# Performance work log

Hardware: AMD Instinct MI355X
Metric: run time of the kernel (lower is better)

Reference implementation:

```python
import jax, jax.numpy as jnp
import numpy as np

BS, D = 4096, 768

def setup_inputs() -> dict:
    key = jax.random.key(0)
    k1, k2 = jax.random.split(key)
    code_vec = jax.random.normal(k1, (BS, D), dtype=jnp.float32)
    nl_vec = jax.random.normal(k2, (BS, D), dtype=jnp.float32)
    return {"code_vec": code_vec, "nl_vec": nl_vec, "bs": BS}

def reference(code_vec, nl_vec, bs):
    # scores[i, j] = <nl_vec[i], code_vec[j]>  -- expressed as a GEMM
    scores = jnp.einsum("nd,md->nm", nl_vec, code_vec)  # [bs, bs]
    # CrossEntropyLoss with labels = arange(bs): mean of -log_softmax diagonal
    logprobs = jax.nn.log_softmax(scores, axis=-1)
    labels = jnp.arange(bs)
    loss = -jnp.mean(logprobs[labels, labels])
    return loss
```

## Files before the change

kernel.cpp:

```cpp
#include <hip/hip_runtime.h>
#include <hip/hip_bf16.h>
#include <math.h>

#define BSZ 4096
#define DIM 768
#define BK 64
#define NTILE (DIM / BK)
#define CSPLIT 16

typedef __attribute__((ext_vector_type(8))) short short8;
typedef __attribute__((ext_vector_type(4))) float f32x4;

__device__ __forceinline__ unsigned short f2bf(float f) {
  unsigned u = __float_as_uint(f);
  u += 0x7fffu + ((u >> 16) & 1u);
  return (unsigned short)(u >> 16);
}

__device__ __forceinline__ void gload16(const void* gp, const void* lp) {
  __builtin_amdgcn_global_load_lds(
      (const __attribute__((address_space(1))) unsigned int*)(size_t)gp,
      (__attribute__((address_space(3))) unsigned int*)(unsigned int)(size_t)lp,
      16, 0, 0);
}

__device__ __forceinline__ short8 lds_ld(const unsigned char* p) {
  return *(const short8*)p;
}

__device__ __forceinline__ void cstore(float* p, float v) {
  __hip_atomic_store(p, v, __ATOMIC_RELAXED, __HIP_MEMORY_SCOPE_AGENT);
}
__device__ __forceinline__ float cload(const float* p) {
  return __hip_atomic_load(p, __ATOMIC_RELAXED, __HIP_MEMORY_SCOPE_AGENT);
}

__global__ void convert_kernel(const float* __restrict__ src0,
                               const float* __restrict__ src1,
                               unsigned short* __restrict__ dst0,
                               unsigned short* __restrict__ dst1,
                               unsigned int* __restrict__ cnt)
{
  if (blockIdx.x == 0 && threadIdx.x <= CSPLIT) cnt[threadIdx.x] = 0u;
  const int n4 = (BSZ * DIM) / 4;
  int i = blockIdx.x * blockDim.x + threadIdx.x;
  const float* src;
  unsigned short* dst;
  if (i < n4) { src = src0; dst = dst0; }
  else        { src = src1; dst = dst1; i -= n4; }
  float4 v = *reinterpret_cast<const float4*>(src + (size_t)i * 4);
  ushort4 o;
  o.x = f2bf(v.x); o.y = f2bf(v.y); o.z = f2bf(v.z); o.w = f2bf(v.w);
  *reinterpret_cast<ushort4*>(dst + (size_t)i * 4) = o;
}

__global__ __launch_bounds__(512, 2)
void gemm_lse_kernel(const unsigned short* __restrict__ A,
                     const unsigned short* __restrict__ B,
                     float* __restrict__ pm, float* __restrict__ ps,
                     float* __restrict__ diag,
                     float* __restrict__ partial,
                     unsigned int* __restrict__ cnt,
                     float* __restrict__ out)
{
  __shared__ alignas(16) unsigned char smem[131072];
  const int tid  = threadIdx.x;
  const int w    = tid >> 6;
  const int lane = tid & 63;
  const int lr   = lane & 15;
  const int hi   = lane >> 4;
  const int wm   = w >> 2;
  const int wn   = w & 3;

  const int id  = blockIdx.y * 16 + blockIdx.x;
  const int xcd = id & 7, sq = id >> 3;
  const int bx  = ((xcd & 3) << 2) | (sq & 3);
  const int by  = ((xcd >> 2) << 3) | (sq >> 2);
  const int i0 = bx << 8;
  const int j0 = by << 8;

  const int fb0 = (hi ^ (lr & 7)) << 4;
  const int fb1 = ((4 + hi) ^ (lr & 7)) << 4;
  const int arowb = (wm * 128 + lr) * 128;
  const int browb = (wn * 64 + lr) * 128;

  const int srow = tid >> 3;
  const int gcol = ((tid & 7) ^ (srow & 7)) << 3;
  const unsigned short* pA = A + (size_t)(i0 + srow) * DIM + gcol;
  const unsigned short* pB = B + (size_t)(j0 + srow) * DIM + gcol;
  const int ldsbase = w << 10;

  f32x4 acc[8][4];
#pragma unroll
  for (int m = 0; m < 8; ++m)
#pragma unroll
    for (int n = 0; n < 4; ++n)
      acc[m][n] = (f32x4){0.f, 0.f, 0.f, 0.f};

#pragma unroll
  for (int q = 0; q < 4; ++q) {
    gload16(pA + (size_t)(q * 64) * DIM, smem + q * 8192 + ldsbase);
    gload16(pB + (size_t)(q * 64) * DIM, smem + 65536 + q * 8192 + ldsbase);
  }
  asm volatile("s_waitcnt vmcnt(0)" ::: "memory");
  __builtin_amdgcn_s_barrier();

#pragma unroll 2
  for (int u = 0; u < NTILE; ++u) {
    const int c = u & 1;
    const unsigned char* la = smem + c * 32768;
    const unsigned char* lb = smem + 65536 + c * 32768;
    unsigned char* na = smem + (c ^ 1) * 32768;
    unsigned char* nb = smem + 65536 + (c ^ 1) * 32768;
    const bool st = (u + 1 < NTILE);
    const size_t kn = (size_t)(u + 1) * BK;

    short8 aF[4], bF[4];

#pragma unroll
    for (int n = 0; n < 4; ++n) bF[n] = lds_ld(lb + browb + n * 2048 + fb0);
#pragma unroll
    for (int m = 0; m < 4; ++m) aF[m] = lds_ld(la + arowb + m * 2048 + fb0);
    if (st) {
      gload16(pB + kn,                     nb + ldsbase);
      gload16(pB + (size_t) 64 * DIM + kn, nb +     8192 + ldsbase);
      gload16(pB + (size_t)128 * DIM + kn, nb + 2 * 8192 + ldsbase);
      gload16(pB + (size_t)192 * DIM + kn, nb + 3 * 8192 + ldsbase);
      gload16(pA + kn,                     na + ldsbase);
      gload16(pA + (size_t)128 * DIM + kn, na + 2 * 8192 + ldsbase);
    }
    __builtin_amdgcn_s_barrier();
    asm volatile("s_waitcnt lgkmcnt(0)" ::: "memory");
    __builtin_amdgcn_s_setprio(1);
#pragma unroll
    for (int m = 0; m < 4; ++m)
#pragma unroll
      for (int n = 0; n < 4; ++n)
        acc[m][n] = __builtin_amdgcn_mfma_f32_16x16x32_bf16(aF[m], bF[n], acc[m][n], 0, 0, 0);
    __builtin_amdgcn_s_setprio(0);
    if (st) asm volatile("s_waitcnt vmcnt(6)" ::: "memory");
    else    asm volatile("s_waitcnt vmcnt(0)" ::: "memory");
    __builtin_amdgcn_s_barrier();

#pragma unroll
    for (int m = 0; m < 4; ++m) aF[m] = lds_ld(la + arowb + (4 + m) * 2048 + fb0);
    if (st) {
      gload16(pA + (size_t) 64 * DIM + kn, na +     8192 + ldsbase);
      gload16(pA + (size_t)192 * DIM + kn, na + 3 * 8192 + ldsbase);
    }
    __builtin_amdgcn_s_barrier();
    asm volatile("s_waitcnt lgkmcnt(0)" ::: "memory");
    __builtin_amdgcn_s_setprio(1);
#pragma unroll
    for (int m = 0; m < 4; ++m)
#pragma unroll
      for (int n = 0; n < 4; ++n)
        acc[4 + m][n] = __builtin_amdgcn_mfma_f32_16x16x32_bf16(aF[m], bF[n], acc[4 + m][n], 0, 0, 0);
    __builtin_amdgcn_s_setprio(0);
    __builtin_amdgcn_s_barrier();

#pragma unroll
    for (int n = 0; n < 4; ++n) bF[n] = lds_ld(lb + browb + n * 2048 + fb1);
#pragma unroll
    for (int m = 0; m < 4; ++m) aF[m] = lds_ld(la + arowb + m * 2048 + fb1);
    __builtin_amdgcn_s_barrier();
    asm volatile("s_waitcnt lgkmcnt(0)" ::: "memory");
    __builtin_amdgcn_s_setprio(1);
#pragma unroll
    for (int m = 0; m < 4; ++m)
#pragma unroll
      for (int n = 0; n < 4; ++n)
        acc[m][n] = __builtin_amdgcn_mfma_f32_16x16x32_bf16(aF[m], bF[n], acc[m][n], 0, 0, 0);
    __builtin_amdgcn_s_setprio(0);
    __builtin_amdgcn_s_barrier();

#pragma unroll
    for (int m = 0; m < 4; ++m) aF[m] = lds_ld(la + arowb + (4 + m) * 2048 + fb1);
    __builtin_amdgcn_s_barrier();
    asm volatile("s_waitcnt lgkmcnt(0)" ::: "memory");
    __builtin_amdgcn_s_setprio(1);
#pragma unroll
    for (int m = 0; m < 4; ++m)
#pragma unroll
      for (int n = 0; n < 4; ++n)
        acc[4 + m][n] = __builtin_amdgcn_mfma_f32_16x16x32_bf16(aF[m], bF[n], acc[4 + m][n], 0, 0, 0);
    __builtin_amdgcn_s_setprio(0);
    if (st) asm volatile("s_waitcnt vmcnt(2)" ::: "memory");
    __builtin_amdgcn_s_barrier();
  }

  __syncthreads();

  if (i0 == j0) {
#pragma unroll
    for (int m = 0; m < 8; ++m)
#pragma unroll
      for (int n = 0; n < 4; ++n)
#pragma unroll
        for (int rr = 0; rr < 4; ++rr) {
          const int rl = wm * 128 + m * 16 + (hi << 2) + rr;
          const int cl = wn * 64 + n * 16 + lr;
          if (rl == cl) cstore(&diag[i0 + rl], acc[m][n][rr]);
        }
  }

  float* redm = (float*)smem;
  float* reds = (float*)(smem + 4096);

#pragma unroll
  for (int m = 0; m < 8; ++m) {
    float mx[4], sm[4];
#pragma unroll
    for (int rr = 0; rr < 4; ++rr) {
      float v = fmaxf(fmaxf(acc[m][0][rr], acc[m][1][rr]),
                      fmaxf(acc[m][2][rr], acc[m][3][rr]));
      mx[rr] = v;
    }
#pragma unroll
    for (int sh = 1; sh < 16; sh <<= 1)
#pragma unroll
      for (int rr = 0; rr < 4; ++rr)
        mx[rr] = fmaxf(mx[rr], __shfl_xor(mx[rr], sh, 64));
#pragma unroll
    for (int rr = 0; rr < 4; ++rr) {
      float s = 0.f;
#pragma unroll
      for (int n = 0; n < 4; ++n) s += __expf(acc[m][n][rr] - mx[rr]);
      sm[rr] = s;
    }
#pragma unroll
    for (int sh = 1; sh < 16; sh <<= 1)
#pragma unroll
      for (int rr = 0; rr < 4; ++rr)
        sm[rr] += __shfl_xor(sm[rr], sh, 64);
    if (lr == 0) {
#pragma unroll
      for (int rr = 0; rr < 4; ++rr) {
        const int rl = wm * 128 + m * 16 + (hi << 2) + rr;
        redm[(wn << 8) + rl] = mx[rr];
        reds[(wn << 8) + rl] = sm[rr];
      }
    }
  }
  __syncthreads();

  if (tid < 256) {
    float m = redm[tid];
#pragma unroll
    for (int v = 1; v < 4; ++v) m = fmaxf(m, redm[(v << 8) + tid]);
    float s = 0.f;
#pragma unroll
    for (int v = 0; v < 4; ++v) s += reds[(v << 8) + tid] * __expf(redm[(v << 8) + tid] - m);
    cstore(&pm[(size_t)by * BSZ + i0 + tid], m);
    cstore(&ps[(size_t)by * BSZ + i0 + tid], s);
  }

  asm volatile("s_waitcnt vmcnt(0)" ::: "memory");
  __syncthreads();
  __shared__ unsigned int sord;
  if (tid == 0) sord = atomicAdd(&cnt[bx], 1u);
  __syncthreads();
  if (sord == CSPLIT - 1) {
    float val = 0.f;
    if (tid < 256) {
      const int row = i0 + tid;
      float mv[CSPLIT];
      float m = -INFINITY;
#pragma unroll
      for (int c = 0; c < CSPLIT; ++c) {
        mv[c] = cload(&pm[(size_t)c * BSZ + row]);
        m = fmaxf(m, mv[c]);
      }
      float s = 0.f;
#pragma unroll
      for (int c = 0; c < CSPLIT; ++c)
        s += cload(&ps[(size_t)c * BSZ + row]) * __expf(mv[c] - m);
      val = (m + __logf(s)) - cload(&diag[row]);
    }
    float* red2 = (float*)smem;
    red2[tid] = val;
    __syncthreads();
    for (int off = 256; off > 0; off >>= 1) {
      if (tid < off) red2[tid] += red2[tid + off];
      __syncthreads();
    }
    if (tid == 0) {
      cstore(&partial[bx], red2[0]);
      asm volatile("s_waitcnt vmcnt(0)" ::: "memory");
      unsigned int d = atomicAdd(&cnt[CSPLIT], 1u);
      if (d == CSPLIT - 1) {
        float s = 0.f;
        for (int i = 0; i < CSPLIT; ++i) s += cload(&partial[i]);
        out[0] = s / (float)BSZ;
      }
    }
  }
}

extern "C" void kernel_launch(void* const* d_in, const int* in_sizes, int n_in,
                              void* d_out, int out_size, void* d_ws, size_t ws_size,
                              hipStream_t stream) {
  const float* code = (const float*)d_in[0];
  const float* nl   = (const float*)d_in[1];
  float* out = (float*)d_out;

  char* ws = (char*)d_ws;
  unsigned short* Abf = (unsigned short*)ws;
  unsigned short* Bbf = (unsigned short*)(ws + (size_t)BSZ * DIM * 2);
  float* pm   = (float*)(ws + (size_t)BSZ * DIM * 4);
  float* ps   = pm + (size_t)CSPLIT * BSZ;
  float* diag = ps + (size_t)CSPLIT * BSZ;
  float* partial = diag + BSZ;
  unsigned int* cnt = (unsigned int*)(partial + CSPLIT);

  const int n4 = (BSZ * DIM) / 4;
  convert_kernel<<<(2 * n4) / 256, 256, 0, stream>>>(nl, code, Abf, Bbf, cnt);

  dim3 grid(BSZ / 256, BSZ / 256);
  gemm_lse_kernel<<<grid, 512, 0, stream>>>(Abf, Bbf, pm, ps, diag, partial, cnt, out);
}
```

Baseline: 47.34 us.

## Fuse fp32-to-bf16 conversion into GEMM loads via register staging

Removes the separate conversion kernel and has the GEMM read fp32 inputs straight from global memory into registers. It converts them to bf16 and writes them swizzled into LDS between MFMA phases, and the counter reset becomes a memset. This drops a kernel launch and the write and re-read of the bf16 copies. In exchange each tile now reads twice as many bytes from global memory, 16 blocks re-read each tile, and direct-to-LDS loads are replaced by register staging, which raises register pressure and adds VALU conversion work inside the main loop.

```diff
diff --git a/kernel.cpp b/kernel.cpp
--- a/kernel.cpp
+++ b/kernel.cpp
@@ -17,17 +17,19 @@
   return (unsigned short)(u >> 16);
 }
 
-__device__ __forceinline__ void gload16(const void* gp, const void* lp) {
-  __builtin_amdgcn_global_load_lds(
-      (const __attribute__((address_space(1))) unsigned int*)(size_t)gp,
-      (__attribute__((address_space(3))) unsigned int*)(unsigned int)(size_t)lp,
-      16, 0, 0);
-}
-
 __device__ __forceinline__ short8 lds_ld(const unsigned char* p) {
   return *(const short8*)p;
 }
 
+__device__ __forceinline__ void cvt_write(unsigned char* dst, f32x4 a, f32x4 b) {
+  short8 o;
+  o[0] = (short)f2bf(a[0]); o[1] = (short)f2bf(a[1]);
+  o[2] = (short)f2bf(a[2]); o[3] = (short)f2bf(a[3]);
+  o[4] = (short)f2bf(b[0]); o[5] = (short)f2bf(b[1]);
+  o[6] = (short)f2bf(b[2]); o[7] = (short)f2bf(b[3]);
+  *(short8*)dst = o;
+}
+
 __device__ __forceinline__ void cstore(float* p, float v) {
   __hip_atomic_store(p, v, __ATOMIC_RELAXED, __HIP_MEMORY_SCOPE_AGENT);
 }
@@ -35,28 +37,9 @@
   return __hip_atomic_load(p, __ATOMIC_RELAXED, __HIP_MEMORY_SCOPE_AGENT);
 }
 
-__global__ void convert_kernel(const float* __restrict__ src0,
-                               const float* __restrict__ src1,
-                               unsigned short* __restrict__ dst0,
-                               unsigned short* __restrict__ dst1,
-                               unsigned int* __restrict__ cnt)
-{
-  if (blockIdx.x == 0 && threadIdx.x <= CSPLIT) cnt[threadIdx.x] = 0u;
-  const int n4 = (BSZ * DIM) / 4;
-  int i = blockIdx.x * blockDim.x + threadIdx.x;
-  const float* src;
-  unsigned short* dst;
-  if (i < n4) { src = src0; dst = dst0; }
-  else        { src = src1; dst = dst1; i -= n4; }
-  float4 v = *reinterpret_cast<const float4*>(src + (size_t)i * 4);
-  ushort4 o;
-  o.x = f2bf(v.x); o.y = f2bf(v.y); o.z = f2bf(v.z); o.w = f2bf(v.w);
-  *reinterpret_cast<ushort4*>(dst + (size_t)i * 4) = o;
-}
-
 __global__ __launch_bounds__(512, 2)
-void gemm_lse_kernel(const unsigned short* __restrict__ A,
-                     const unsigned short* __restrict__ B,
+void gemm_lse_kernel(const float* __restrict__ Af,
+                     const float* __restrict__ Bf,
                      float* __restrict__ pm, float* __restrict__ ps,
                      float* __restrict__ diag,
                      float* __restrict__ partial,
@@ -85,10 +68,10 @@
   const int browb = (wn * 64 + lr) * 128;
 
   const int srow = tid >> 3;
-  const int gcol = ((tid & 7) ^ (srow & 7)) << 3;
-  const unsigned short* pA = A + (size_t)(i0 + srow) * DIM + gcol;
-  const unsigned short* pB = B + (size_t)(j0 + srow) * DIM + gcol;
-  const int ldsbase = w << 10;
+  const int seg  = tid & 7;
+  const float* gA = Af + (size_t)(i0 + srow) * DIM + (seg << 3);
+  const float* gB = Bf + (size_t)(j0 + srow) * DIM + (seg << 3);
+  const int swz = srow * 128 + ((seg ^ (srow & 7)) << 4);
 
   f32x4 acc[8][4];
 #pragma unroll
@@ -97,12 +80,21 @@
     for (int n = 0; n < 4; ++n)
       acc[m][n] = (f32x4){0.f, 0.f, 0.f, 0.f};
 
+  f32x4 ar[8], br[8];
+
+#pragma unroll
+  for (int q = 0; q < 4; ++q)
+#pragma unroll
+    for (int h = 0; h < 2; ++h) {
+      br[q * 2 + h] = *reinterpret_cast<const f32x4*>(gB + (size_t)(q * 64) * DIM + h * 4);
+      ar[q * 2 + h] = *reinterpret_cast<const f32x4*>(gA + (size_t)(q * 64) * DIM + h * 4);
+    }
 #pragma unroll
   for (int q = 0; q < 4; ++q) {
-    gload16(pA + (size_t)(q * 64) * DIM, smem + q * 8192 + ldsbase);
-    gload16(pB + (size_t)(q * 64) * DIM, smem + 65536 + q * 8192 + ldsbase);
-  }
-  asm volatile("s_waitcnt vmcnt(0)" ::: "memory");
+    cvt_write(smem + 65536 + q * 8192 + swz, br[2 * q], br[2 * q + 1]);
+    cvt_write(smem +         q * 8192 + swz, ar[2 * q], ar[2 * q + 1]);
+  }
+  asm volatile("s_waitcnt lgkmcnt(0)" ::: "memory");
   __builtin_amdgcn_s_barrier();
 
 #pragma unroll 2
@@ -122,12 +114,11 @@
 #pragma unroll
     for (int m = 0; m < 4; ++m) aF[m] = lds_ld(la + arowb + m * 2048 + fb0);
     if (st) {
-      gload16(pB + kn,                     nb + ldsbase);
-      gload16(pB + (size_t) 64 * DIM + kn, nb +     8192 + ldsbase);
-      gload16(pB + (size_t)128 * DIM + kn, nb + 2 * 8192 + ldsbase);
-      gload16(pB + (size_t)192 * DIM + kn, nb + 3 * 8192 + ldsbase);
-      gload16(pA + kn,                     na + ldsbase);
-      gload16(pA + (size_t)128 * DIM + kn, na + 2 * 8192 + ldsbase);
+#pragma unroll
+      for (int q = 0; q < 4; ++q)
+#pragma unroll
+        for (int h = 0; h < 2; ++h)
+          br[q * 2 + h] = *reinterpret_cast<const f32x4*>(gB + (size_t)(q * 64) * DIM + kn + h * 4);
     }
     __builtin_amdgcn_s_barrier();
     asm volatile("s_waitcnt lgkmcnt(0)" ::: "memory");
@@ -138,15 +129,16 @@
       for (int n = 0; n < 4; ++n)
         acc[m][n] = __builtin_amdgcn_mfma_f32_16x16x32_bf16(aF[m], bF[n], acc[m][n], 0, 0, 0);
     __builtin_amdgcn_s_setprio(0);
-    if (st) asm volatile("s_waitcnt vmcnt(6)" ::: "memory");
-    else    asm volatile("s_waitcnt vmcnt(0)" ::: "memory");
     __builtin_amdgcn_s_barrier();
 
 #pragma unroll
     for (int m = 0; m < 4; ++m) aF[m] = lds_ld(la + arowb + (4 + m) * 2048 + fb0);
     if (st) {
-      gload16(pA + (size_t) 64 * DIM + kn, na +     8192 + ldsbase);
-      gload16(pA + (size_t)192 * DIM + kn, na + 3 * 8192 + ldsbase);
+#pragma unroll
+      for (int q = 0; q < 4; ++q)
+#pragma unroll
+        for (int h = 0; h < 2; ++h)
+          ar[q * 2 + h] = *reinterpret_cast<const f32x4*>(gA + (size_t)(q * 64) * DIM + kn + h * 4);
     }
     __builtin_amdgcn_s_barrier();
     asm volatile("s_waitcnt lgkmcnt(0)" ::: "memory");
@@ -172,6 +164,11 @@
       for (int n = 0; n < 4; ++n)
         acc[m][n] = __builtin_amdgcn_mfma_f32_16x16x32_bf16(aF[m], bF[n], acc[m][n], 0, 0, 0);
     __builtin_amdgcn_s_setprio(0);
+    if (st) {
+#pragma unroll
+      for (int q = 0; q < 4; ++q)
+        cvt_write(nb + q * 8192 + swz, br[2 * q], br[2 * q + 1]);
+    }
     __builtin_amdgcn_s_barrier();
 
 #pragma unroll
@@ -185,7 +182,12 @@
       for (int n = 0; n < 4; ++n)
         acc[4 + m][n] = __builtin_amdgcn_mfma_f32_16x16x32_bf16(aF[m], bF[n], acc[4 + m][n], 0, 0, 0);
     __builtin_amdgcn_s_setprio(0);
-    if (st) asm volatile("s_waitcnt vmcnt(2)" ::: "memory");
+    if (st) {
+#pragma unroll
+      for (int q = 0; q < 4; ++q)
+        cvt_write(na + q * 8192 + swz, ar[2 * q], ar[2 * q + 1]);
+    }
+    asm volatile("s_waitcnt lgkmcnt(0)" ::: "memory");
     __builtin_amdgcn_s_barrier();
   }
 
@@ -305,17 +307,14 @@
   float* out = (float*)d_out;
 
   char* ws = (char*)d_ws;
-  unsigned short* Abf = (unsigned short*)ws;
-  unsigned short* Bbf = (unsigned short*)(ws + (size_t)BSZ * DIM * 2);
-  float* pm   = (float*)(ws + (size_t)BSZ * DIM * 4);
+  float* pm   = (float*)ws;
   float* ps   = pm + (size_t)CSPLIT * BSZ;
   float* diag = ps + (size_t)CSPLIT * BSZ;
   float* partial = diag + BSZ;
   unsigned int* cnt = (unsigned int*)(partial + CSPLIT);
 
-  const int n4 = (BSZ * DIM) / 4;
-  convert_kernel<<<(2 * n4) / 256, 256, 0, stream>>>(nl, code, Abf, Bbf, cnt);
+  hipMemsetAsync(cnt, 0, (CSPLIT + 1) * sizeof(unsigned int), stream);
 
   dim3 grid(BSZ / 256, BSZ / 256);
-  gemm_lse_kernel<<<grid, 512, 0, stream>>>(Abf, Bbf, pm, ps, diag, partial, cnt, out);
-}
+  gemm_lse_kernel<<<grid, 512, 0, stream>>>(nl, code, pm, ps, diag, partial, cnt, out);
+}
```

After: 112.7 us. 2.38x slower.

## Shrink GEMM tile to 128x256 to double block count and remap grid

Applied to the files above, without the earlier changes.

Halves the row tile from 256 to 128. The grid grows to 32x16 blocks, each with a smaller accumulator set and half as much A in LDS. The block-to-XCD swizzle is remapped for the new grid, the diagonal extraction is adjusted for offset tiles, and the final reduction now runs over 32 row panels. The aim is better CU utilisation and occupancy from having more blocks. The cost is lower arithmetic intensity per block and more redundant B loads.

```diff
diff --git a/kernel.cpp b/kernel.cpp
--- a/kernel.cpp
+++ b/kernel.cpp
@@ -7,6 +7,7 @@
 #define BK 64
 #define NTILE (DIM / BK)
 #define CSPLIT 16
+#define NPANEL 32
 
 typedef __attribute__((ext_vector_type(8))) short short8;
 typedef __attribute__((ext_vector_type(4))) float f32x4;
@@ -41,7 +42,7 @@
                                unsigned short* __restrict__ dst1,
                                unsigned int* __restrict__ cnt)
 {
-  if (blockIdx.x == 0 && threadIdx.x <= CSPLIT) cnt[threadIdx.x] = 0u;
+  if (blockIdx.x == 0 && threadIdx.x <= NPANEL) cnt[threadIdx.x] = 0u;
   const int n4 = (BSZ * DIM) / 4;
   int i = blockIdx.x * blockDim.x + threadIdx.x;
   const float* src;
@@ -63,7 +64,7 @@
                      unsigned int* __restrict__ cnt,
                      float* __restrict__ out)
 {
-  __shared__ alignas(16) unsigned char smem[131072];
+  __shared__ alignas(16) unsigned char smem[98304];
   const int tid  = threadIdx.x;
   const int w    = tid >> 6;
   const int lane = tid & 63;
@@ -72,16 +73,20 @@
   const int wm   = w >> 2;
   const int wn   = w & 3;
 
-  const int id  = blockIdx.y * 16 + blockIdx.x;
-  const int xcd = id & 7, sq = id >> 3;
-  const int bx  = ((xcd & 3) << 2) | (sq & 3);
-  const int by  = ((xcd >> 2) << 3) | (sq >> 2);
-  const int i0 = bx << 8;
-  const int j0 = by << 8;
+  const int g   = blockIdx.y * 32 + blockIdx.x;
+  const int xcd = g & 7;
+  const int t   = g >> 3;
+  const int rnd = t >> 5;
+  const int s   = t & 31;
+  const int bxl = s & 7, byl = s >> 3;
+  const int bx  = ((xcd & 3) << 3) | bxl;
+  const int by  = ((xcd >> 2) << 3) | (rnd << 2) | byl;
+  const int i0  = bx << 7;
+  const int j0  = by << 8;
 
   const int fb0 = (hi ^ (lr & 7)) << 4;
   const int fb1 = ((4 + hi) ^ (lr & 7)) << 4;
-  const int arowb = (wm * 128 + lr) * 128;
+  const int arowb = (wm * 64 + lr) * 128;
   const int browb = (wn * 64 + lr) * 128;
 
   const int srow = tid >> 3;
@@ -90,28 +95,28 @@
   const unsigned short* pB = B + (size_t)(j0 + srow) * DIM + gcol;
   const int ldsbase = w << 10;
 
-  f32x4 acc[8][4];
-#pragma unroll
-  for (int m = 0; m < 8; ++m)
+  f32x4 acc[4][4];
+#pragma unroll
+  for (int m = 0; m < 4; ++m)
 #pragma unroll
     for (int n = 0; n < 4; ++n)
       acc[m][n] = (f32x4){0.f, 0.f, 0.f, 0.f};
 
-#pragma unroll
-  for (int q = 0; q < 4; ++q) {
-    gload16(pA + (size_t)(q * 64) * DIM, smem + q * 8192 + ldsbase);
-    gload16(pB + (size_t)(q * 64) * DIM, smem + 65536 + q * 8192 + ldsbase);
-  }
+  gload16(pA,                      smem +        ldsbase);
+  gload16(pA + (size_t)64 * DIM,   smem + 8192 + ldsbase);
+#pragma unroll
+  for (int q = 0; q < 4; ++q)
+    gload16(pB + (size_t)(q * 64) * DIM, smem + 32768 + q * 8192 + ldsbase);
   asm volatile("s_waitcnt vmcnt(0)" ::: "memory");
   __builtin_amdgcn_s_barrier();
 
 #pragma unroll 2
   for (int u = 0; u < NTILE; ++u) {
     const int c = u & 1;
-    const unsigned char* la = smem + c * 32768;
-    const unsigned char* lb = smem + 65536 + c * 32768;
-    unsigned char* na = smem + (c ^ 1) * 32768;
-    unsigned char* nb = smem + 65536 + (c ^ 1) * 32768;
+    const unsigned char* la = smem + c * 16384;
+    const unsigned char* lb = smem + 32768 + c * 32768;
+    unsigned char* na = smem + (c ^ 1) * 16384;
+    unsigned char* nb = smem + 32768 + (c ^ 1) * 32768;
     const bool st = (u + 1 < NTILE);
     const size_t kn = (size_t)(u + 1) * BK;
 
@@ -127,7 +132,7 @@
       gload16(pB + (size_t)128 * DIM + kn, nb + 2 * 8192 + ldsbase);
       gload16(pB + (size_t)192 * DIM + kn, nb + 3 * 8192 + ldsbase);
       gload16(pA + kn,                     na + ldsbase);
-      gload16(pA + (size_t)128 * DIM + kn, na + 2 * 8192 + ldsbase);
+      gload16(pA + (size_t) 64 * DIM + kn, na +     8192 + ldsbase);
     }
     __builtin_amdgcn_s_barrier();
     asm volatile("s_waitcnt lgkmcnt(0)" ::: "memory");
@@ -138,25 +143,6 @@
       for (int n = 0; n < 4; ++n)
         acc[m][n] = __builtin_amdgcn_mfma_f32_16x16x32_bf16(aF[m], bF[n], acc[m][n], 0, 0, 0);
     __builtin_amdgcn_s_setprio(0);
-    if (st) asm volatile("s_waitcnt vmcnt(6)" ::: "memory");
-    else    asm volatile("s_waitcnt vmcnt(0)" ::: "memory");
-    __builtin_amdgcn_s_barrier();
-
-#pragma unroll
-    for (int m = 0; m < 4; ++m) aF[m] = lds_ld(la + arowb + (4 + m) * 2048 + fb0);
-    if (st) {
-      gload16(pA + (size_t) 64 * DIM + kn, na +     8192 + ldsbase);
-      gload16(pA + (size_t)192 * DIM + kn, na + 3 * 8192 + ldsbase);
-    }
-    __builtin_amdgcn_s_barrier();
-    asm volatile("s_waitcnt lgkmcnt(0)" ::: "memory");
-    __builtin_amdgcn_s_setprio(1);
-#pragma unroll
-    for (int m = 0; m < 4; ++m)
-#pragma unroll
-      for (int n = 0; n < 4; ++n)
-        acc[4 + m][n] = __builtin_amdgcn_mfma_f32_16x16x32_bf16(aF[m], bF[n], acc[4 + m][n], 0, 0, 0);
-    __builtin_amdgcn_s_setprio(0);
     __builtin_amdgcn_s_barrier();
 
 #pragma unroll
@@ -172,43 +158,31 @@
       for (int n = 0; n < 4; ++n)
         acc[m][n] = __builtin_amdgcn_mfma_f32_16x16x32_bf16(aF[m], bF[n], acc[m][n], 0, 0, 0);
     __builtin_amdgcn_s_setprio(0);
-    __builtin_amdgcn_s_barrier();
-
-#pragma unroll
-    for (int m = 0; m < 4; ++m) aF[m] = lds_ld(la + arowb + (4 + m) * 2048 + fb1);
-    __builtin_amdgcn_s_barrier();
-    asm volatile("s_waitcnt lgkmcnt(0)" ::: "memory");
-    __builtin_amdgcn_s_setprio(1);
+    asm volatile("s_waitcnt vmcnt(0)" ::: "memory");
+    __builtin_amdgcn_s_barrier();
+  }
+
+  __syncthreads();
+
+  const int dof = i0 - j0;
+  if (dof >= 0 && dof < 256) {
 #pragma unroll
     for (int m = 0; m < 4; ++m)
 #pragma unroll
       for (int n = 0; n < 4; ++n)
-        acc[4 + m][n] = __builtin_amdgcn_mfma_f32_16x16x32_bf16(aF[m], bF[n], acc[4 + m][n], 0, 0, 0);
-    __builtin_amdgcn_s_setprio(0);
-    if (st) asm volatile("s_waitcnt vmcnt(2)" ::: "memory");
-    __builtin_amdgcn_s_barrier();
-  }
-
-  __syncthreads();
-
-  if (i0 == j0) {
-#pragma unroll
-    for (int m = 0; m < 8; ++m)
-#pragma unroll
-      for (int n = 0; n < 4; ++n)
 #pragma unroll
         for (int rr = 0; rr < 4; ++rr) {
-          const int rl = wm * 128 + m * 16 + (hi << 2) + rr;
+          const int rl = wm * 64 + m * 16 + (hi << 2) + rr;
           const int cl = wn * 64 + n * 16 + lr;
-          if (rl == cl) cstore(&diag[i0 + rl], acc[m][n][rr]);
+          if (cl == rl + dof) cstore(&diag[i0 + rl], acc[m][n][rr]);
         }
   }
 
   float* redm = (float*)smem;
-  float* reds = (float*)(smem + 4096);
-
-#pragma unroll
-  for (int m = 0; m < 8; ++m) {
+  float* reds = (float*)(smem + 2048);
+
+#pragma unroll
+  for (int m = 0; m < 4; ++m) {
     float mx[4], sm[4];
 #pragma unroll
     for (int rr = 0; rr < 4; ++rr) {
@@ -236,21 +210,21 @@
     if (lr == 0) {
 #pragma unroll
       for (int rr = 0; rr < 4; ++rr) {
-        const int rl = wm * 128 + m * 16 + (hi << 2) + rr;
-        redm[(wn << 8) + rl] = mx[rr];
-        reds[(wn << 8) + rl] = sm[rr];
+        const int rl = wm * 64 + m * 16 + (hi << 2) + rr;
+        redm[(wn << 7) + rl] = mx[rr];
+        reds[(wn << 7) + rl] = sm[rr];
       }
     }
   }
   __syncthreads();
 
-  if (tid < 256) {
+  if (tid < 128) {
     float m = redm[tid];
 #pragma unroll
-    for (int v = 1; v < 4; ++v) m = fmaxf(m, redm[(v << 8) + tid]);
+    for (int v = 1; v < 4; ++v) m = fmaxf(m, redm[(v << 7) + tid]);
     float s = 0.f;
 #pragma unroll
-    for (int v = 0; v < 4; ++v) s += reds[(v << 8) + tid] * __expf(redm[(v << 8) + tid] - m);
+    for (int v = 0; v < 4; ++v) s += reds[(v << 7) + tid] * __expf(redm[(v << 7) + tid] - m);
     cstore(&pm[(size_t)by * BSZ + i0 + tid], m);
     cstore(&ps[(size_t)by * BSZ + i0 + tid], s);
   }
@@ -262,7 +236,7 @@
   __syncthreads();
   if (sord == CSPLIT - 1) {
     float val = 0.f;
-    if (tid < 256) {
+    if (tid < 128) {
       const int row = i0 + tid;
       float mv[CSPLIT];
       float m = -INFINITY;
@@ -287,10 +261,10 @@
     if (tid == 0) {
       cstore(&partial[bx], red2[0]);
       asm volatile("s_waitcnt vmcnt(0)" ::: "memory");
-      unsigned int d = atomicAdd(&cnt[CSPLIT], 1u);
-      if (d == CSPLIT - 1) {
+      unsigned int d = atomicAdd(&cnt[NPANEL], 1u);
+      if (d == NPANEL - 1) {
         float s = 0.f;
-        for (int i = 0; i < CSPLIT; ++i) s += cload(&partial[i]);
+        for (int i = 0; i < NPANEL; ++i) s += cload(&partial[i]);
         out[0] = s / (float)BSZ;
       }
     }
@@ -311,11 +285,11 @@
   float* ps   = pm + (size_t)CSPLIT * BSZ;
   float* diag = ps + (size_t)CSPLIT * BSZ;
   float* partial = diag + BSZ;
-  unsigned int* cnt = (unsigned int*)(partial + CSPLIT);
+  unsigned int* cnt = (unsigned int*)(partial + NPANEL);
 
   const int n4 = (BSZ * DIM) / 4;
   convert_kernel<<<(2 * n4) / 256, 256, 0, stream>>>(nl, code, Abf, Bbf, cnt);
 
-  dim3 grid(BSZ / 256, BSZ / 256);
+  dim3 grid(BSZ / 128, BSZ / 256);
   gemm_lse_kernel<<<grid, 512, 0, stream>>>(Abf, Bbf, pm, ps, diag, partial, cnt, out);
 }
```

Result: slower. 52.26 us (+10.4%).

## Replace barrier-phased K loop with per-wave staggered sub-phases and single barrier

Applied to the files above, without the earlier changes.

The inner K-tile loop no longer uses lockstep phases separated by many workgroup barriers. Each wave now walks four sub-phases (M half by K chunk) in a rotated order chosen by its wave index, so LDS reads and MFMA bursts of different waves are staggered. All global-to-LDS prefetches for the next tile are issued at once, followed by one vmcnt(0) wait and a single barrier per tile. This removes barrier stalls, but the prefetch now waits for completion within the same tile rather than being spread out, and the compiler schedules LDS waits implicitly. Halving role rotation means B fragments get reloaded when kc changes mid-order.

```diff
diff --git a/kernel.cpp b/kernel.cpp
--- a/kernel.cpp
+++ b/kernel.cpp
@@ -71,6 +71,7 @@
   const int hi   = lane >> 4;
   const int wm   = w >> 2;
   const int wn   = w & 3;
+  const int role = (w & 1) << 1;
 
   const int id  = blockIdx.y * 16 + blockIdx.x;
   const int xcd = id & 7, sq = id >> 3;
@@ -118,74 +119,39 @@
     short8 aF[4], bF[4];
 
 #pragma unroll
-    for (int n = 0; n < 4; ++n) bF[n] = lds_ld(lb + browb + n * 2048 + fb0);
-#pragma unroll
-    for (int m = 0; m < 4; ++m) aF[m] = lds_ld(la + arowb + m * 2048 + fb0);
-    if (st) {
-      gload16(pB + kn,                     nb + ldsbase);
-      gload16(pB + (size_t) 64 * DIM + kn, nb +     8192 + ldsbase);
-      gload16(pB + (size_t)128 * DIM + kn, nb + 2 * 8192 + ldsbase);
-      gload16(pB + (size_t)192 * DIM + kn, nb + 3 * 8192 + ldsbase);
-      gload16(pA + kn,                     na + ldsbase);
-      gload16(pA + (size_t)128 * DIM + kn, na + 2 * 8192 + ldsbase);
-    }
-    __builtin_amdgcn_s_barrier();
-    asm volatile("s_waitcnt lgkmcnt(0)" ::: "memory");
-    __builtin_amdgcn_s_setprio(1);
-#pragma unroll
-    for (int m = 0; m < 4; ++m)
-#pragma unroll
-      for (int n = 0; n < 4; ++n)
-        acc[m][n] = __builtin_amdgcn_mfma_f32_16x16x32_bf16(aF[m], bF[n], acc[m][n], 0, 0, 0);
-    __builtin_amdgcn_s_setprio(0);
-    if (st) asm volatile("s_waitcnt vmcnt(6)" ::: "memory");
-    else    asm volatile("s_waitcnt vmcnt(0)" ::: "memory");
-    __builtin_amdgcn_s_barrier();
-
-#pragma unroll
-    for (int m = 0; m < 4; ++m) aF[m] = lds_ld(la + arowb + (4 + m) * 2048 + fb0);
-    if (st) {
-      gload16(pA + (size_t) 64 * DIM + kn, na +     8192 + ldsbase);
-      gload16(pA + (size_t)192 * DIM + kn, na + 3 * 8192 + ldsbase);
-    }
-    __builtin_amdgcn_s_barrier();
-    asm volatile("s_waitcnt lgkmcnt(0)" ::: "memory");
-    __builtin_amdgcn_s_setprio(1);
-#pragma unroll
-    for (int m = 0; m < 4; ++m)
-#pragma unroll
-      for (int n = 0; n < 4; ++n)
-        acc[4 + m][n] = __builtin_amdgcn_mfma_f32_16x16x32_bf16(aF[m], bF[n], acc[4 + m][n], 0, 0, 0);
-    __builtin_amdgcn_s_setprio(0);
-    __builtin_amdgcn_s_barrier();
-
-#pragma unroll
-    for (int n = 0; n < 4; ++n) bF[n] = lds_ld(lb + browb + n * 2048 + fb1);
-#pragma unroll
-    for (int m = 0; m < 4; ++m) aF[m] = lds_ld(la + arowb + m * 2048 + fb1);
-    __builtin_amdgcn_s_barrier();
-    asm volatile("s_waitcnt lgkmcnt(0)" ::: "memory");
-    __builtin_amdgcn_s_setprio(1);
-#pragma unroll
-    for (int m = 0; m < 4; ++m)
-#pragma unroll
-      for (int n = 0; n < 4; ++n)
-        acc[m][n] = __builtin_amdgcn_mfma_f32_16x16x32_bf16(aF[m], bF[n], acc[m][n], 0, 0, 0);
-    __builtin_amdgcn_s_setprio(0);
-    __builtin_amdgcn_s_barrier();
-
-#pragma unroll
-    for (int m = 0; m < 4; ++m) aF[m] = lds_ld(la + arowb + (4 + m) * 2048 + fb1);
-    __builtin_amdgcn_s_barrier();
-    asm volatile("s_waitcnt lgkmcnt(0)" ::: "memory");
-    __builtin_amdgcn_s_setprio(1);
-#pragma unroll
-    for (int m = 0; m < 4; ++m)
-#pragma unroll
-      for (int n = 0; n < 4; ++n)
-        acc[4 + m][n] = __builtin_amdgcn_mfma_f32_16x16x32_bf16(aF[m], bF[n], acc[4 + m][n], 0, 0, 0);
-    __builtin_amdgcn_s_setprio(0);
-    if (st) asm volatile("s_waitcnt vmcnt(2)" ::: "memory");
+    for (int pp = 0; pp < 4; ++pp) {
+      const int p  = (pp + role) & 3;
+      const int mh = p & 1;
+      const int kc = p >> 1;
+      const int fbp = kc ? fb1 : fb0;
+
+      if (pp == 0 || pp == 2) {
+#pragma unroll
+        for (int n = 0; n < 4; ++n) bF[n] = lds_ld(lb + browb + n * 2048 + fbp);
+      }
+#pragma unroll
+      for (int m = 0; m < 4; ++m)
+        aF[m] = lds_ld(la + arowb + (mh * 4 + m) * 2048 + fbp);
+
+      if (pp == 0 && st) {
+#pragma unroll
+        for (int q = 0; q < 4; ++q) {
+          gload16(pB + (size_t)(q * 64) * DIM + kn, nb + q * 8192 + ldsbase);
+          gload16(pA + (size_t)(q * 64) * DIM + kn, na + q * 8192 + ldsbase);
+        }
+      }
+
+      __builtin_amdgcn_s_setprio(1);
+#pragma unroll
+      for (int m = 0; m < 4; ++m)
+#pragma unroll
+        for (int n = 0; n < 4; ++n)
+          acc[mh * 4 + m][n] =
+              __builtin_amdgcn_mfma_f32_16x16x32_bf16(aF[m], bF[n], acc[mh * 4 + m][n], 0, 0, 0);
+      __builtin_amdgcn_s_setprio(0);
+    }
+
+    asm volatile("s_waitcnt vmcnt(0)" ::: "memory");
     __builtin_amdgcn_s_barrier();
   }
 
```

Result: faster. 45.38 us (median of 3 runs) (-4.1%).
